# Kernel optimization log

Measured on AMD Instinct MI355X. Metric: run time of the kernel, lower is better.

Reference implementation:

```python
import jax, jax.numpy as jnp
import numpy as np

N_NODES = 100000
N_EDGES = 600000
N_GRAPHS = 64
BN_EPS = 1e-5


def setup_inputs() -> dict:
    key = jax.random.key(0)
    ks = jax.random.split(key, 32)
    inp = {
        "x": jax.random.normal(ks[0], (N_NODES, 128), dtype=jnp.float32),
        "edge_index": jax.random.randint(ks[1], (2, N_EDGES), 0, N_NODES, dtype=jnp.int64),
        "batch": jnp.sort(jax.random.randint(ks[2], (N_NODES,), 0, N_GRAPHS, dtype=jnp.int64)),
    }
    dims = [(128, 64, 64), (64, 64, 64), (64, 64, 96)]  # (in, hid, out) per GIN layer
    ki = 3
    for i, (d_in, d_hid, d_out) in enumerate(dims):
        inp[f"l{i}_w1"] = jax.random.normal(ks[ki], (d_in, d_hid), dtype=jnp.float32) * 0.05; ki += 1
        inp[f"l{i}_b1"] = jnp.zeros((d_hid,), dtype=jnp.float32)
        inp[f"l{i}_w2"] = jax.random.normal(ks[ki], (d_hid, d_out), dtype=jnp.float32) * 0.05; ki += 1
        inp[f"l{i}_b2"] = jnp.zeros((d_out,), dtype=jnp.float32)
        inp[f"bn{i}_g"] = jax.random.uniform(ks[ki], (d_out,), minval=0.5, maxval=1.5, dtype=jnp.float32); ki += 1
        inp[f"bn{i}_b"] = jax.random.normal(ks[ki], (d_out,), dtype=jnp.float32) * 0.05; ki += 1
        inp[f"bn{i}_m"] = jax.random.normal(ks[ki], (d_out,), dtype=jnp.float32) * 0.05; ki += 1
        inp[f"bn{i}_v"] = jax.random.uniform(ks[ki], (d_out,), minval=0.5, maxval=1.5, dtype=jnp.float32); ki += 1
    return inp


def _gin_layer(x, src, dst, w1, b1, w2, b2, g, bb, m, v):
    # GINConv (eps=0): h_i = MLP(x_i + sum_{j: j->i} x_j)
    aggr = jax.ops.segment_sum(x[src], dst, num_segments=N_NODES)
    h = x + aggr
    h = jax.nn.relu(h @ w1 + b1) @ w2 + b2
    # eval-mode BatchNorm1d + ReLU
    h = (h - m) * jax.lax.rsqrt(v + BN_EPS) * g + bb
    return jax.nn.relu(h)


def reference(x, edge_index, batch,
              l0_w1, l0_b1, l0_w2, l0_b2, bn0_g, bn0_b, bn0_m, bn0_v,
              l1_w1, l1_b1, l1_w2, l1_b2, bn1_g, bn1_b, bn1_m, bn1_v,
              l2_w1, l2_b1, l2_w2, l2_b2, bn2_g, bn2_b, bn2_m, bn2_v):
    src, dst = edge_index[0], edge_index[1]
    h = _gin_layer(x, src, dst, l0_w1, l0_b1, l0_w2, l0_b2, bn0_g, bn0_b, bn0_m, bn0_v)
    h = _gin_layer(h, src, dst, l1_w1, l1_b1, l1_w2, l1_b2, bn1_g, bn1_b, bn1_m, bn1_v)
    h = _gin_layer(h, src, dst, l2_w1, l2_b1, l2_w2, l2_b2, bn2_g, bn2_b, bn2_m, bn2_v)
    # global mean pool over graphs
    sums = jax.ops.segment_sum(h, batch, num_segments=N_GRAPHS)
    counts = jax.ops.segment_sum(jnp.ones((h.shape[0],), dtype=h.dtype), batch, num_segments=N_GRAPHS)
    return sums / jnp.maximum(counts, 1.0)[:, None]
```

## Files before the change

### kernel.cpp

```cpp
#include <hip/hip_runtime.h>

#define N_NODES 100000
#define N_GRAPHS 64
#define N_EDGES 600000
#define BN_EPS 1e-5f

typedef unsigned short bf16_t;

__device__ __forceinline__ unsigned short f2bf(float f) {
    unsigned int u = __float_as_uint(f);
    u += 0x7FFF + ((u >> 16) & 1);
    return (unsigned short)(u >> 16);
}
__device__ __forceinline__ uint2 pack4(float a, float b, float c, float d) {
    uint2 p;
    p.x = (unsigned)f2bf(a) | ((unsigned)f2bf(b) << 16);
    p.y = (unsigned)f2bf(c) | ((unsigned)f2bf(d) << 16);
    return p;
}
__device__ __forceinline__ void bf8_acc(uint4 q, float* acc) {
    acc[0] += __uint_as_float(q.x << 16);
    acc[1] += __uint_as_float(q.x & 0xFFFF0000u);
    acc[2] += __uint_as_float(q.y << 16);
    acc[3] += __uint_as_float(q.y & 0xFFFF0000u);
    acc[4] += __uint_as_float(q.z << 16);
    acc[5] += __uint_as_float(q.z & 0xFFFF0000u);
    acc[6] += __uint_as_float(q.w << 16);
    acc[7] += __uint_as_float(q.w & 0xFFFF0000u);
}

__global__ void deg_hist_kernel(const int* __restrict__ dst,
                                int* __restrict__ deg, int n_edges) {
    int e = blockIdx.x * blockDim.x + threadIdx.x;
    if (e < n_edges) atomicAdd(&deg[dst[e]], 1);
}

__global__ __launch_bounds__(1024)
void scan_fused_kernel(const int* __restrict__ deg, int* __restrict__ rowptr,
                       int* __restrict__ agg, int n, int total) {
    __shared__ int s[1024];
    __shared__ int s2[128];
    __shared__ int offset_sh;
    const int b = blockIdx.x;
    const int i = b * 1024 + threadIdx.x;
    int v = (i < n) ? deg[i] : 0;
    s[threadIdx.x] = v;
    __syncthreads();
    for (int off = 1; off < 1024; off <<= 1) {
        int t = (threadIdx.x >= (unsigned)off) ? s[threadIdx.x - off] : 0;
        __syncthreads();
        s[threadIdx.x] += t;
        __syncthreads();
    }
    if (threadIdx.x == 1023) atomicExch(&agg[b], s[1023]);
    if (threadIdx.x < b) {
        int val;
        do { val = atomicAdd(&agg[threadIdx.x], 0); } while (val == -1);
        s2[threadIdx.x] = val;
    }
    __syncthreads();
    if (threadIdx.x == 0) {
        int off = 0;
        for (int k = 0; k < b; ++k) off += s2[k];
        offset_sh = off;
    }
    __syncthreads();
    const int off = offset_sh;
    if (i < n) rowptr[i] = off + s[threadIdx.x] - v;
    else if (i == n) rowptr[n] = total;
}

__global__ __launch_bounds__(256)
void fill_pre_kernel(const int* __restrict__ src, const int* __restrict__ dst,
                     const int* __restrict__ rowptr, int* __restrict__ cursor,
                     int* __restrict__ eids, const int* __restrict__ batch,
                     int* __restrict__ gstart,
                     const float* __restrict__ x, const float* __restrict__ w1T,
                     bf16_t* __restrict__ y, int n_edges, int n_nodes) {
    __shared__ float w1s[64 * 128];
    const int bq = blockIdx.x / 5, br = blockIdx.x % 5;

    if (br < 3) {
        int e = (bq * 3 + br) * 256 + threadIdx.x;
        if (e < n_edges) {
            int t = dst[e];
            int pos = rowptr[t] + atomicAdd(&cursor[t], 1);
            eids[pos] = src[e];
        }
        if (e < n_nodes) {
            if (e == 0) {
                for (int g = 0; g <= batch[0]; ++g) gstart[g] = 0;
            } else {
                int b0 = batch[e - 1], b1 = batch[e];
                for (int g = b0 + 1; g <= b1; ++g) gstart[g] = e;
            }
            if (e == n_nodes - 1) {
                for (int g = batch[e] + 1; g <= N_GRAPHS; ++g) gstart[g] = n_nodes;
            }
        }
        return;
    }

    const int gb = bq * 2 + (br - 3);
    const long base = (long)gb * 64;
    if (base >= n_nodes) return;
    const int tid = threadIdx.x;

    const float4* gw1 = (const float4*)w1T;
    for (int i4 = tid; i4 < 16 * 128; i4 += 256) {
        int row = i4 >> 5, k4 = i4 & 31;
        *(float4*)&w1s[row * 128 + ((k4 ^ ((row >> 2) & 7)) << 2)] = gw1[i4];
    }
    __syncthreads();

    const int jg = tid & 15, ng = tid >> 4, xw = jg & 7;
    const float* wp = &w1s[(jg * 4) * 128];
    const float4* xv = (const float4*)x;
    long r[4];
    #pragma unroll
    for (int i = 0; i < 4; ++i) {
        long rr = base + ng * 4 + i;
        r[i] = (rr < n_nodes) ? rr : (n_nodes - 1);
    }
    float acc[4][4] = {};
    #pragma unroll 4
    for (int k4 = 0; k4 < 32; ++k4) {
        const int ko = (k4 ^ xw) << 2;
        float4 w0 = *(const float4*)&wp[0 * 128 + ko];
        float4 w1v = *(const float4*)&wp[1 * 128 + ko];
        float4 w2v = *(const float4*)&wp[2 * 128 + ko];
        float4 w3v = *(const float4*)&wp[3 * 128 + ko];
        #pragma unroll
        for (int i = 0; i < 4; ++i) {
            float4 a = xv[r[i] * 32 + k4];
            acc[i][0] = fmaf(a.x, w0.x, fmaf(a.y, w0.y, fmaf(a.z, w0.z, fmaf(a.w, w0.w, acc[i][0]))));
            acc[i][1] = fmaf(a.x, w1v.x, fmaf(a.y, w1v.y, fmaf(a.z, w1v.z, fmaf(a.w, w1v.w, acc[i][1]))));
            acc[i][2] = fmaf(a.x, w2v.x, fmaf(a.y, w2v.y, fmaf(a.z, w2v.z, fmaf(a.w, w2v.w, acc[i][2]))));
            acc[i][3] = fmaf(a.x, w3v.x, fmaf(a.y, w3v.y, fmaf(a.z, w3v.z, fmaf(a.w, w3v.w, acc[i][3]))));
        }
    }
    #pragma unroll
    for (int i = 0; i < 4; ++i) {
        long n = base + ng * 4 + i;
        if (n < n_nodes) {
            *(uint2*)(y + n * 64 + jg * 4) = pack4(acc[i][0], acc[i][1], acc[i][2], acc[i][3]);
        }
    }
}

struct LayerPrep {
    const float *w1, *w2, *b2, *g, *bb, *m, *v;
    float *w1T, *w2sT, *bias2;
    int DIN, DOUT;
};
struct PrepAll { LayerPrep l[3]; };

__global__ void prep_all_kernel(PrepAll pa, int* __restrict__ deg,
                                int* __restrict__ cursor, float* __restrict__ out_zero,
                                int* __restrict__ agg) {
    LayerPrep P = pa.l[blockIdx.y];
    int i = blockIdx.x * blockDim.x + threadIdx.x;
    if (blockIdx.y == 0) {
        int stride = gridDim.x * blockDim.x;
        for (int k = i; k < N_NODES; k += stride) { deg[k] = 0; cursor[k] = 0; }
        for (int k = i; k < N_GRAPHS * 96; k += stride) out_zero[k] = 0.0f;
        if (i < 128) agg[i] = -1;
    }
    if (i < 64 * P.DIN) {
        int j = i / P.DIN, k = i % P.DIN;
        P.w1T[i] = P.w1[k * 64 + j];
    }
    int i2 = i - 64 * P.DIN;
    if (i2 >= 0 && i2 < P.DOUT * 64) {
        int c = i2 / 64, j = i2 % 64;
        float s = P.g[c] * rsqrtf(P.v[c] + BN_EPS);
        P.w2sT[i2] = P.w2[j * P.DOUT + c] * s;
    }
    int i3 = i2 - P.DOUT * 64;
    if (i3 >= 0 && i3 < P.DOUT) {
        float s = P.g[i3] * rsqrtf(P.v[i3] + BN_EPS);
        P.bias2[i3] = (P.b2[i3] - P.m[i3]) * s + P.bb[i3];
    }
}

__global__ __launch_bounds__(256)
void gather64_kernel(const bf16_t* __restrict__ y, const int* __restrict__ rowptr,
                     const int* __restrict__ eids, const float* __restrict__ b1,
                     float* __restrict__ t, int n_nodes) {
    int node = blockIdx.x * 32 + (threadIdx.x >> 3);
    if (node >= n_nodes) return;
    int f = threadIdx.x & 7;
    const uint4* yv = (const uint4*)y;
    float acc[8] = {};
    bf8_acc(yv[(long)node * 8 + f], acc);
    int b = rowptr[node], e = rowptr[node + 1];
    int i = b;
    for (; i + 3 < e; i += 4) {
        int s0 = eids[i], s1 = eids[i + 1], s2 = eids[i + 2], s3 = eids[i + 3];
        uint4 q0 = yv[(long)s0 * 8 + f];
        uint4 q1 = yv[(long)s1 * 8 + f];
        uint4 q2 = yv[(long)s2 * 8 + f];
        uint4 q3 = yv[(long)s3 * 8 + f];
        bf8_acc(q0, acc); bf8_acc(q1, acc); bf8_acc(q2, acc); bf8_acc(q3, acc);
    }
    for (; i < e; ++i) bf8_acc(yv[(long)eids[i] * 8 + f], acc);

    float4 b0 = ((const float4*)b1)[f * 2];
    float4 b1v = ((const float4*)b1)[f * 2 + 1];
    float4 o0, o1;
    o0.x = fmaxf(acc[0] + b0.x, 0.0f);
    o0.y = fmaxf(acc[1] + b0.y, 0.0f);
    o0.z = fmaxf(acc[2] + b0.z, 0.0f);
    o0.w = fmaxf(acc[3] + b0.w, 0.0f);
    o1.x = fmaxf(acc[4] + b1v.x, 0.0f);
    o1.y = fmaxf(acc[5] + b1v.y, 0.0f);
    o1.z = fmaxf(acc[6] + b1v.z, 0.0f);
    o1.w = fmaxf(acc[7] + b1v.w, 0.0f);
    ((float4*)t)[(long)node * 16 + f * 2] = o0;
    ((float4*)t)[(long)node * 16 + f * 2 + 1] = o1;
}

__global__ __launch_bounds__(256)
void fused_mid_kernel(const float* __restrict__ t, const float* __restrict__ w2sT,
                      const float* __restrict__ bias2, const float* __restrict__ w1nT,
                      bf16_t* __restrict__ ynext, int n_nodes) {
    constexpr int SS = 68;
    __shared__ float sT[64 * SS];
    __shared__ float wbuf[64 * 64];
    const int tid = threadIdx.x;
    const long base = (long)blockIdx.x * 64;

    const float4* gw2 = (const float4*)w2sT;
    for (int i4 = tid; i4 < 16 * 64; i4 += 256) {
        int row = i4 >> 4, k4 = i4 & 15;
        *(float4*)&wbuf[row * 64 + ((k4 ^ ((row >> 2) & 7)) << 2)] = gw2[i4];
    }
    __syncthreads();

    const int jg = tid & 15, ng = tid >> 4, xw = jg & 7;
    const float4* tv = (const float4*)(t + base * 64);

    float h[4][4];
    {
        const float* wp = &wbuf[(jg * 4) * 64];
        float acc[4][4] = {};
        #pragma unroll 4
        for (int k4 = 0; k4 < 16; ++k4) {
            const int ko = (k4 ^ xw) << 2;
            float4 w0 = *(const float4*)&wp[0 * 64 + ko];
            float4 w1v = *(const float4*)&wp[1 * 64 + ko];
            float4 w2v = *(const float4*)&wp[2 * 64 + ko];
            float4 w3v = *(const float4*)&wp[3 * 64 + ko];
            #pragma unroll
            for (int i = 0; i < 4; ++i) {
                float4 a = tv[(ng * 4 + i) * 16 + k4];
                acc[i][0] = fmaf(a.x, w0.x, fmaf(a.y, w0.y, fmaf(a.z, w0.z, fmaf(a.w, w0.w, acc[i][0]))));
                acc[i][1] = fmaf(a.x, w1v.x, fmaf(a.y, w1v.y, fmaf(a.z, w1v.z, fmaf(a.w, w1v.w, acc[i][1]))));
                acc[i][2] = fmaf(a.x, w2v.x, fmaf(a.y, w2v.y, fmaf(a.z, w2v.z, fmaf(a.w, w2v.w, acc[i][2]))));
                acc[i][3] = fmaf(a.x, w3v.x, fmaf(a.y, w3v.y, fmaf(a.z, w3v.z, fmaf(a.w, w3v.w, acc[i][3]))));
            }
        }
        float4 bv = *(const float4*)&bias2[jg * 4];
        #pragma unroll
        for (int i = 0; i < 4; ++i) {
            h[i][0] = fmaxf(acc[i][0] + bv.x, 0.0f);
            h[i][1] = fmaxf(acc[i][1] + bv.y, 0.0f);
            h[i][2] = fmaxf(acc[i][2] + bv.z, 0.0f);
            h[i][3] = fmaxf(acc[i][3] + bv.w, 0.0f);
        }
    }
    __syncthreads();

    #pragma unroll
    for (int i = 0; i < 4; ++i) {
        float4 hv = {h[i][0], h[i][1], h[i][2], h[i][3]};
        *(float4*)&sT[(ng * 4 + i) * SS + jg * 4] = hv;
    }
    const float4* gw1n = (const float4*)w1nT;
    for (int i4 = tid; i4 < 16 * 64; i4 += 256) {
        int row = i4 >> 4, k4 = i4 & 15;
        *(float4*)&wbuf[row * 64 + ((k4 ^ ((row >> 2) & 7)) << 2)] = gw1n[i4];
    }
    __syncthreads();

    {
        const float* ap = &sT[(ng * 4) * SS];
        const float* wp = &wbuf[(jg * 4) * 64];
        float acc[4][4] = {};
        #pragma unroll 4
        for (int k4 = 0; k4 < 16; ++k4) {
            const int ko = (k4 ^ xw) << 2;
            float4 w0 = *(const float4*)&wp[0 * 64 + ko];
            float4 w1v = *(const float4*)&wp[1 * 64 + ko];
            float4 w2v = *(const float4*)&wp[2 * 64 + ko];
            float4 w3v = *(const float4*)&wp[3 * 64 + ko];
            #pragma unroll
            for (int i = 0; i < 4; ++i) {
                float4 a = *(const float4*)&ap[i * SS + k4 * 4];
                acc[i][0] = fmaf(a.x, w0.x, fmaf(a.y, w0.y, fmaf(a.z, w0.z, fmaf(a.w, w0.w, acc[i][0]))));
                acc[i][1] = fmaf(a.x, w1v.x, fmaf(a.y, w1v.y, fmaf(a.z, w1v.z, fmaf(a.w, w1v.w, acc[i][1]))));
                acc[i][2] = fmaf(a.x, w2v.x, fmaf(a.y, w2v.y, fmaf(a.z, w2v.z, fmaf(a.w, w2v.w, acc[i][2]))));
                acc[i][3] = fmaf(a.x, w3v.x, fmaf(a.y, w3v.y, fmaf(a.z, w3v.z, fmaf(a.w, w3v.w, acc[i][3]))));
            }
        }
        #pragma unroll
        for (int i = 0; i < 4; ++i) {
            long n = base + ng * 4 + i;
            if (n < n_nodes) {
                *(uint2*)(ynext + n * 64 + jg * 4) = pack4(acc[i][0], acc[i][1], acc[i][2], acc[i][3]);
            }
        }
    }
}

__global__ __launch_bounds__(256)
void fused_final_kernel(const float* __restrict__ t, const float* __restrict__ w2sT,
                        const float* __restrict__ bias2, const int* __restrict__ batch,
                        const int* __restrict__ gstart, float* __restrict__ out,
                        int n_nodes) {
    constexpr int CPT = 6;
    __shared__ float w2s[96 * 64];
    const int tid = threadIdx.x;
    const long base = (long)blockIdx.x * 64;

    const float4* gw2 = (const float4*)w2sT;
    for (int i4 = tid; i4 < 96 * 16; i4 += 256) {
        int row = i4 >> 4, k4 = i4 & 15;
        *(float4*)&w2s[row * 64 + ((k4 ^ ((row / CPT) & 7)) << 2)] = gw2[i4];
    }
    __syncthreads();

    const int cg_ = tid & 15, ng = tid >> 4, xw = cg_ & 7;
    const float4* tv = (const float4*)(t + base * 64);
    const float* wp = &w2s[(cg_ * CPT) * 64];
    float acc[4][CPT] = {};
    #pragma unroll 4
    for (int k4 = 0; k4 < 16; ++k4) {
        const int ko = (k4 ^ xw) << 2;
        float4 wv[CPT];
        #pragma unroll
        for (int c = 0; c < CPT; ++c) wv[c] = *(const float4*)&wp[c * 64 + ko];
        #pragma unroll
        for (int i = 0; i < 4; ++i) {
            float4 h = tv[(ng * 4 + i) * 16 + k4];
            #pragma unroll
            for (int c = 0; c < CPT; ++c)
                acc[i][c] = fmaf(h.x, wv[c].x, fmaf(h.y, wv[c].y, fmaf(h.z, wv[c].z, fmaf(h.w, wv[c].w, acc[i][c]))));
        }
    }
    float bv[CPT];
    #pragma unroll
    for (int c = 0; c < CPT; ++c) bv[c] = bias2[cg_ * CPT + c];
    __syncthreads();
    #pragma unroll
    for (int i = 0; i < 4; ++i) {
        long n = base + ng * 4 + i;
        float* hp = &w2s[(ng * 4 + i) * 96 + cg_ * CPT];
        if (n < n_nodes) {
            #pragma unroll
            for (int c = 0; c < CPT; ++c) hp[c] = fmaxf(acc[i][c] + bv[c], 0.0f);
        } else {
            #pragma unroll
            for (int c = 0; c < CPT; ++c) hp[c] = 0.0f;
        }
    }
    __syncthreads();

    if (tid < 96) {
        int limit = (int)((n_nodes - base < 64) ? (n_nodes - base) : 64);
        int gcur = batch[base];
        float s = 0.0f;
        for (int r = 0; r < limit; ++r) {
            int g = batch[base + r];
            if (g != gcur) {
                float inv = 1.0f / fmaxf((float)(gstart[gcur + 1] - gstart[gcur]), 1.0f);
                atomicAdd(&out[gcur * 96 + tid], s * inv);
                s = 0.0f;
                gcur = g;
            }
            s += w2s[r * 96 + tid];
        }
        float inv = 1.0f / fmaxf((float)(gstart[gcur + 1] - gstart[gcur]), 1.0f);
        atomicAdd(&out[gcur * 96 + tid], s * inv);
    }
}

static inline int cdiv_l(long a, int b) { return (int)((a + b - 1) / b); }

extern "C" void kernel_launch(void* const* d_in, const int* in_sizes, int n_in,
                              void* d_out, int out_size, void* d_ws, size_t ws_size,
                              hipStream_t stream) {
    const float* x     = (const float*)d_in[0];
    const int*   ei    = (const int*)d_in[1];
    const int*   src   = ei;
    const int*   dst   = ei + N_EDGES;
    const int*   batch = (const int*)d_in[2];

    const float* P[3][8];
    int p = 3;
    for (int l = 0; l < 3; ++l)
        for (int q = 0; q < 8; ++q)
            P[l][q] = (const float*)d_in[p++];

    const long NP = N_NODES + 128;
    char* wsb   = (char*)d_ws;
    bf16_t* yA  = (bf16_t*)wsb;
    bf16_t* yB  = yA + NP * 64;
    float* gB   = (float*)(yB + NP * 64);
    float* q    = gB + NP * 64;
    float* w1T[3], *w2sT[3], *bias2[3];
    for (int l = 0; l < 3; ++l) {
        w1T[l] = q;   q += 64 * 128;
        w2sT[l] = q;  q += 96 * 64;
        bias2[l] = q; q += 96;
    }
    int* gstart   = (int*)q;
    int* deg      = gstart + 72;
    int* cursor   = deg + N_NODES;
    int* partials = cursor + N_NODES;
    int* rowptr   = partials + 128;
    int* eids     = rowptr + (N_NODES + 1);

    const int B = 256;
    const int DIN[3]  = {128, 64, 64};
    const int DOUT[3] = {64, 64, 96};

    PrepAll pa;
    for (int l = 0; l < 3; ++l) {
        pa.l[l].w1 = P[l][0]; pa.l[l].w2 = P[l][2]; pa.l[l].b2 = P[l][3];
        pa.l[l].g = P[l][4];  pa.l[l].bb = P[l][5]; pa.l[l].m = P[l][6];
        pa.l[l].v = P[l][7];
        pa.l[l].w1T = w1T[l]; pa.l[l].w2sT = w2sT[l]; pa.l[l].bias2 = bias2[l];
        pa.l[l].DIN = DIN[l]; pa.l[l].DOUT = DOUT[l];
    }
    dim3 pgrid(cdiv_l(64 * 128 + 96 * 64 + 96, B), 3);
    prep_all_kernel<<<pgrid, B, 0, stream>>>(pa, deg, cursor, (float*)d_out, partials);

    deg_hist_kernel<<<cdiv_l(N_EDGES, B), B, 0, stream>>>(dst, deg, N_EDGES);
    int nblk = cdiv_l(N_NODES + 1, 1024);
    scan_fused_kernel<<<nblk, 1024, 0, stream>>>(deg, rowptr, partials, N_NODES, N_EDGES);

    const int nfill  = cdiv_l(N_EDGES, B);
    const int ngemm  = cdiv_l(N_NODES, 64);
    const int ngrp_f = cdiv_l(nfill, 3);
    const int ngrp_g = cdiv_l(ngemm, 2);
    const int ngroups = (ngrp_f > ngrp_g) ? ngrp_f : ngrp_g;
    fill_pre_kernel<<<ngroups * 5, B, 0, stream>>>(
        src, dst, rowptr, cursor, eids, batch, gstart,
        x, w1T[0], yA, N_EDGES, N_NODES);

    const int ntiles = cdiv_l(N_NODES, 64);
    const int ngather = cdiv_l(N_NODES, 32);

    gather64_kernel<<<ngather, 256, 0, stream>>>(yA, rowptr, eids, P[0][1], gB, N_NODES);
    fused_mid_kernel<<<ntiles, 256, 0, stream>>>(
        gB, w2sT[0], bias2[0], w1T[1], yB, N_NODES);
    gather64_kernel<<<ngather, 256, 0, stream>>>(yB, rowptr, eids, P[1][1], gB, N_NODES);
    fused_mid_kernel<<<ntiles, 256, 0, stream>>>(
        gB, w2sT[1], bias2[1], w1T[2], yA, N_NODES);
    gather64_kernel<<<ngather, 256, 0, stream>>>(yA, rowptr, eids, P[2][1], gB, N_NODES);
    fused_final_kernel<<<ntiles, 256, 0, stream>>>(
        gB, w2sT[2], bias2[2], batch, gstart, (float*)d_out, N_NODES);
}
```

Before: 367.9 us.

## Fuse neighbor gather into per-tile MLP kernels via shared memory

The separate gather kernel that wrote an fp32 intermediate to global memory is removed. Each 64-node MLP tile block now gathers its own neighbor sums into shared memory before running its matmuls, for both the mid and final layers. This drops three launches and the write and read-back of a 100k x 64 fp32 buffer per layer. In exchange, each block does two gather passes with higher shared-memory use, which may lower occupancy and latency hiding for the irregular gathers.

```diff
diff --git a/kernel.cpp b/kernel.cpp
--- a/kernel.cpp
+++ b/kernel.cpp
@@ -27,6 +27,53 @@
     acc[5] += __uint_as_float(q.z & 0xFFFF0000u);
     acc[6] += __uint_as_float(q.w << 16);
     acc[7] += __uint_as_float(q.w & 0xFFFF0000u);
+}
+
+template <int SS>
+__device__ __forceinline__ void gather_tile_to_lds(
+    const bf16_t* __restrict__ y, const int* __restrict__ rowptr,
+    const int* __restrict__ eids, const float* __restrict__ b1,
+    float* sT, long base, int n_nodes, int tid) {
+    const uint4* yv = (const uint4*)y;
+    const int f = tid & 7;
+    float4 b0 = ((const float4*)b1)[f * 2];
+    float4 b1v = ((const float4*)b1)[f * 2 + 1];
+    #pragma unroll
+    for (int pass = 0; pass < 2; ++pass) {
+        int lr = pass * 32 + (tid >> 3);
+        long node = base + lr;
+        float* sp = &sT[lr * SS + f * 8];
+        if (node < n_nodes) {
+            float acc[8] = {};
+            bf8_acc(yv[node * 8 + f], acc);
+            int bgn = rowptr[node], end = rowptr[node + 1];
+            int i = bgn;
+            for (; i + 3 < end; i += 4) {
+                int s0 = eids[i], s1 = eids[i + 1], s2 = eids[i + 2], s3 = eids[i + 3];
+                uint4 q0 = yv[(long)s0 * 8 + f];
+                uint4 q1 = yv[(long)s1 * 8 + f];
+                uint4 q2 = yv[(long)s2 * 8 + f];
+                uint4 q3 = yv[(long)s3 * 8 + f];
+                bf8_acc(q0, acc); bf8_acc(q1, acc); bf8_acc(q2, acc); bf8_acc(q3, acc);
+            }
+            for (; i < end; ++i) bf8_acc(yv[(long)eids[i] * 8 + f], acc);
+            float4 o0, o1;
+            o0.x = fmaxf(acc[0] + b0.x, 0.0f);
+            o0.y = fmaxf(acc[1] + b0.y, 0.0f);
+            o0.z = fmaxf(acc[2] + b0.z, 0.0f);
+            o0.w = fmaxf(acc[3] + b0.w, 0.0f);
+            o1.x = fmaxf(acc[4] + b1v.x, 0.0f);
+            o1.y = fmaxf(acc[5] + b1v.y, 0.0f);
+            o1.z = fmaxf(acc[6] + b1v.z, 0.0f);
+            o1.w = fmaxf(acc[7] + b1v.w, 0.0f);
+            *(float4*)sp = o0;
+            *(float4*)(sp + 4) = o1;
+        } else {
+            float4 z = {0.0f, 0.0f, 0.0f, 0.0f};
+            *(float4*)sp = z;
+            *(float4*)(sp + 4) = z;
+        }
+    }
 }
 
 __global__ void deg_hist_kernel(const int* __restrict__ dst,
@@ -184,46 +231,14 @@
 }
 
 __global__ __launch_bounds__(256)
-void gather64_kernel(const bf16_t* __restrict__ y, const int* __restrict__ rowptr,
-                     const int* __restrict__ eids, const float* __restrict__ b1,
-                     float* __restrict__ t, int n_nodes) {
-    int node = blockIdx.x * 32 + (threadIdx.x >> 3);
-    if (node >= n_nodes) return;
-    int f = threadIdx.x & 7;
-    const uint4* yv = (const uint4*)y;
-    float acc[8] = {};
-    bf8_acc(yv[(long)node * 8 + f], acc);
-    int b = rowptr[node], e = rowptr[node + 1];
-    int i = b;
-    for (; i + 3 < e; i += 4) {
-        int s0 = eids[i], s1 = eids[i + 1], s2 = eids[i + 2], s3 = eids[i + 3];
-        uint4 q0 = yv[(long)s0 * 8 + f];
-        uint4 q1 = yv[(long)s1 * 8 + f];
-        uint4 q2 = yv[(long)s2 * 8 + f];
-        uint4 q3 = yv[(long)s3 * 8 + f];
-        bf8_acc(q0, acc); bf8_acc(q1, acc); bf8_acc(q2, acc); bf8_acc(q3, acc);
-    }
-    for (; i < e; ++i) bf8_acc(yv[(long)eids[i] * 8 + f], acc);
-
-    float4 b0 = ((const float4*)b1)[f * 2];
-    float4 b1v = ((const float4*)b1)[f * 2 + 1];
-    float4 o0, o1;
-    o0.x = fmaxf(acc[0] + b0.x, 0.0f);
-    o0.y = fmaxf(acc[1] + b0.y, 0.0f);
-    o0.z = fmaxf(acc[2] + b0.z, 0.0f);
-    o0.w = fmaxf(acc[3] + b0.w, 0.0f);
-    o1.x = fmaxf(acc[4] + b1v.x, 0.0f);
-    o1.y = fmaxf(acc[5] + b1v.y, 0.0f);
-    o1.z = fmaxf(acc[6] + b1v.z, 0.0f);
-    o1.w = fmaxf(acc[7] + b1v.w, 0.0f);
-    ((float4*)t)[(long)node * 16 + f * 2] = o0;
-    ((float4*)t)[(long)node * 16 + f * 2 + 1] = o1;
-}
-
-__global__ __launch_bounds__(256)
-void fused_mid_kernel(const float* __restrict__ t, const float* __restrict__ w2sT,
-                      const float* __restrict__ bias2, const float* __restrict__ w1nT,
-                      bf16_t* __restrict__ ynext, int n_nodes) {
+void fused_gather_mid_kernel(const bf16_t* __restrict__ y,
+                             const int* __restrict__ rowptr,
+                             const int* __restrict__ eids,
+                             const float* __restrict__ b1,
+                             const float* __restrict__ w2sT,
+                             const float* __restrict__ bias2,
+                             const float* __restrict__ w1nT,
+                             bf16_t* __restrict__ ynext, int n_nodes) {
     constexpr int SS = 68;
     __shared__ float sT[64 * SS];
     __shared__ float wbuf[64 * 64];
@@ -235,10 +250,10 @@
         int row = i4 >> 4, k4 = i4 & 15;
         *(float4*)&wbuf[row * 64 + ((k4 ^ ((row >> 2) & 7)) << 2)] = gw2[i4];
     }
+    gather_tile_to_lds<SS>(y, rowptr, eids, b1, sT, base, n_nodes, tid);
     __syncthreads();
 
     const int jg = tid & 15, ng = tid >> 4, xw = jg & 7;
-    const float4* tv = (const float4*)(t + base * 64);
 
     float h[4][4];
     {
@@ -253,7 +268,7 @@
             float4 w3v = *(const float4*)&wp[3 * 64 + ko];
             #pragma unroll
             for (int i = 0; i < 4; ++i) {
-                float4 a = tv[(ng * 4 + i) * 16 + k4];
+                float4 a = *(const float4*)&sT[(ng * 4 + i) * SS + k4 * 4];
                 acc[i][0] = fmaf(a.x, w0.x, fmaf(a.y, w0.y, fmaf(a.z, w0.z, fmaf(a.w, w0.w, acc[i][0]))));
                 acc[i][1] = fmaf(a.x, w1v.x, fmaf(a.y, w1v.y, fmaf(a.z, w1v.z, fmaf(a.w, w1v.w, acc[i][1]))));
                 acc[i][2] = fmaf(a.x, w2v.x, fmaf(a.y, w2v.y, fmaf(a.z, w2v.z, fmaf(a.w, w2v.w, acc[i][2]))));
@@ -314,12 +329,19 @@
 }
 
 __global__ __launch_bounds__(256)
-void fused_final_kernel(const float* __restrict__ t, const float* __restrict__ w2sT,
-                        const float* __restrict__ bias2, const int* __restrict__ batch,
-                        const int* __restrict__ gstart, float* __restrict__ out,
-                        int n_nodes) {
+void fused_gather_final_kernel(const bf16_t* __restrict__ y,
+                               const int* __restrict__ rowptr,
+                               const int* __restrict__ eids,
+                               const float* __restrict__ b1,
+                               const float* __restrict__ w2sT,
+                               const float* __restrict__ bias2,
+                               const int* __restrict__ batch,
+                               const int* __restrict__ gstart,
+                               float* __restrict__ out, int n_nodes) {
     constexpr int CPT = 6;
+    constexpr int SS = 68;
     __shared__ float w2s[96 * 64];
+    __shared__ float tbuf[64 * SS];
     const int tid = threadIdx.x;
     const long base = (long)blockIdx.x * 64;
 
@@ -328,10 +350,10 @@
         int row = i4 >> 4, k4 = i4 & 15;
         *(float4*)&w2s[row * 64 + ((k4 ^ ((row / CPT) & 7)) << 2)] = gw2[i4];
     }
+    gather_tile_to_lds<SS>(y, rowptr, eids, b1, tbuf, base, n_nodes, tid);
     __syncthreads();
 
     const int cg_ = tid & 15, ng = tid >> 4, xw = cg_ & 7;
-    const float4* tv = (const float4*)(t + base * 64);
     const float* wp = &w2s[(cg_ * CPT) * 64];
     float acc[4][CPT] = {};
     #pragma unroll 4
@@ -342,7 +364,7 @@
         for (int c = 0; c < CPT; ++c) wv[c] = *(const float4*)&wp[c * 64 + ko];
         #pragma unroll
         for (int i = 0; i < 4; ++i) {
-            float4 h = tv[(ng * 4 + i) * 16 + k4];
+            float4 h = *(const float4*)&tbuf[(ng * 4 + i) * SS + k4 * 4];
             #pragma unroll
             for (int c = 0; c < CPT; ++c)
                 acc[i][c] = fmaf(h.x, wv[c].x, fmaf(h.y, wv[c].y, fmaf(h.z, wv[c].z, fmaf(h.w, wv[c].w, acc[i][c]))));
@@ -406,8 +428,7 @@
     char* wsb   = (char*)d_ws;
     bf16_t* yA  = (bf16_t*)wsb;
     bf16_t* yB  = yA + NP * 64;
-    float* gB   = (float*)(yB + NP * 64);
-    float* q    = gB + NP * 64;
+    float* q    = (float*)(yB + NP * 64);
     float* w1T[3], *w2sT[3], *bias2[3];
     for (int l = 0; l < 3; ++l) {
         w1T[l] = q;   q += 64 * 128;
@@ -450,15 +471,12 @@
         x, w1T[0], yA, N_EDGES, N_NODES);
 
     const int ntiles = cdiv_l(N_NODES, 64);
-    const int ngather = cdiv_l(N_NODES, 32);
-
-    gather64_kernel<<<ngather, 256, 0, stream>>>(yA, rowptr, eids, P[0][1], gB, N_NODES);
-    fused_mid_kernel<<<ntiles, 256, 0, stream>>>(
-        gB, w2sT[0], bias2[0], w1T[1], yB, N_NODES);
-    gather64_kernel<<<ngather, 256, 0, stream>>>(yB, rowptr, eids, P[1][1], gB, N_NODES);
-    fused_mid_kernel<<<ntiles, 256, 0, stream>>>(
-        gB, w2sT[1], bias2[1], w1T[2], yA, N_NODES);
-    gather64_kernel<<<ngather, 256, 0, stream>>>(yA, rowptr, eids, P[2][1], gB, N_NODES);
-    fused_final_kernel<<<ntiles, 256, 0, stream>>>(
-        gB, w2sT[2], bias2[2], batch, gstart, (float*)d_out, N_NODES);
-}
+
+    fused_gather_mid_kernel<<<ntiles, 256, 0, stream>>>(
+        yA, rowptr, eids, P[0][1], w2sT[0], bias2[0], w1T[1], yB, N_NODES);
+    fused_gather_mid_kernel<<<ntiles, 256, 0, stream>>>(
+        yB, rowptr, eids, P[1][1], w2sT[1], bias2[1], w1T[2], yA, N_NODES);
+    fused_gather_final_kernel<<<ntiles, 256, 0, stream>>>(
+        yA, rowptr, eids, P[2][1], w2sT[2], bias2[2], batch, gstart,
+        (float*)d_out, N_NODES);
+}
```

Measured after the change: 365.8 us. Within noise of the previous version (-0.6%).
